# Optimization experiments

Measured on AMD Instinct MI355X. Metric: run time of the kernel, lower is better.

Reference implementation:

```python
import jax, jax.numpy as jnp
import numpy as np

B, T, D, H, L = 32, 512, 1024, 1024, 2


def setup_inputs() -> dict:
    key = jax.random.key(0)
    ks = jax.random.split(key, 8)
    s_in = 1.0 / np.sqrt(D)   # approximate orthogonal-init scale
    s_h = 1.0 / np.sqrt(H)
    return {
        "x": jax.random.normal(ks[0], (B, T, D), jnp.float32),
        "hidden": jnp.zeros((L, B, H), jnp.float32),
        "w_ih0": jax.random.normal(ks[1], (3 * H, D), jnp.float32) * s_in,
        "w_hh0": jax.random.normal(ks[2], (3 * H, H), jnp.float32) * s_h,
        "b_ih0": jnp.zeros((3 * H,), jnp.float32),
        "b_hh0": jnp.zeros((3 * H,), jnp.float32),
        "w_ih1": jax.random.normal(ks[3], (3 * H, H), jnp.float32) * s_h,
        "w_hh1": jax.random.normal(ks[4], (3 * H, H), jnp.float32) * s_h,
        "b_ih1": jnp.zeros((3 * H,), jnp.float32),
        "b_hh1": jnp.zeros((3 * H,), jnp.float32),
    }


def _gru_layer(x, h0, w_ih, w_hh, b_ih, b_hh):
    # x: [B,T,Din] -> precompute input projection once (as in source)
    xp = jnp.einsum('btd,gd->btg', x, w_ih) + b_ih        # [B,T,3H]
    xp_t = jnp.swapaxes(xp, 0, 1)                          # [T,B,3H]

    def step(h, xpt):
        hp = h @ w_hh.T + b_hh                             # [B,3H]
        r = jax.nn.sigmoid(xpt[:, :H] + hp[:, :H])
        z = jax.nn.sigmoid(xpt[:, H:2 * H] + hp[:, H:2 * H])
        n = jnp.tanh(xpt[:, 2 * H:] + r * hp[:, 2 * H:])
        h_new = (1 - z) * n + z * h
        return h_new, h_new

    h_last, ys = jax.lax.scan(step, h0, xp_t)              # ys: [T,B,H]
    return jnp.swapaxes(ys, 0, 1), h_last


def reference(x, hidden, w_ih0, w_hh0, b_ih0, b_hh0,
              w_ih1, w_hh1, b_ih1, b_hh1):
    y0, h0 = _gru_layer(x, hidden[0], w_ih0, w_hh0, b_ih0, b_hh0)
    y1, h1 = _gru_layer(y0, hidden[1], w_ih1, w_hh1, b_ih1, b_hh1)
    # dropout rates are 0.0 (eval semantics) -> identity
    return y1, jnp.stack([h0, h1], axis=0)
```

## Files before the change

kernel.cpp:

```cpp
#include <hip/hip_runtime.h>
#include <hip/hip_bf16.h>

#define NB 32
#define NT 512
#define NH 1024
#define G3 3072
#define NWG 128
#define PK_LDS (98304 + 16384 + 8192)

typedef __attribute__((ext_vector_type(8))) short short8;
typedef __attribute__((ext_vector_type(4))) float f32x4;
typedef __attribute__((ext_vector_type(4))) unsigned short us4;

static __device__ __forceinline__ unsigned short f2bf(float f) {
    union { float f; unsigned u; } v; v.f = f;
    if ((v.u & 0x7fffffffu) > 0x7f800000u) return (unsigned short)((v.u >> 16) | 0x0040u);
    unsigned u = v.u + 0x7fffu + ((v.u >> 16) & 1u);
    return (unsigned short)(u >> 16);
}

__global__ __launch_bounds__(256) void cvt_bf16_v4(const float4* __restrict__ src,
                                                   us4* __restrict__ dst, int n4) {
    for (int i = blockIdx.x * 256 + threadIdx.x; i < n4; i += gridDim.x * 256) {
        float4 v = src[i];
        us4 o;
        o.x = f2bf(v.x); o.y = f2bf(v.y); o.z = f2bf(v.z); o.w = f2bf(v.w);
        dst[i] = o;
    }
}

__global__ __launch_bounds__(256) void txp_x(const float4* __restrict__ x, us4* __restrict__ xt) {
    const int total = NT * NB * 256;
    for (int i = blockIdx.x * 256 + threadIdx.x; i < total; i += gridDim.x * 256) {
        int b = i / (NT * 256);
        int rem = i - b * (NT * 256);
        int t = rem >> 8;
        int d4 = rem & 255;
        float4 v = x[i];
        us4 o;
        o.x = f2bf(v.x); o.y = f2bf(v.y); o.z = f2bf(v.z); o.w = f2bf(v.w);
        xt[((size_t)t * NB + b) * 256 + d4] = o;
    }
}

__global__ __launch_bounds__(256) void init_h(const float* __restrict__ hid,
                                              float* __restrict__ h0f, unsigned short* __restrict__ h0b,
                                              float* __restrict__ h1f, unsigned short* __restrict__ h1b) {
    int i = blockIdx.x * 256 + threadIdx.x;
    float v0 = hid[i];
    float v1 = hid[NB * NH + i];
    h0f[i] = v0; h0b[i] = f2bf(v0);
    h1f[i] = v1; h1b[i] = f2bf(v1);
}

__global__ __launch_bounds__(256, 1) void gru_persistent(
    const unsigned short* __restrict__ xt,
    unsigned short* __restrict__ y0b,
    const unsigned short* __restrict__ wih0, const unsigned short* __restrict__ whh0,
    const unsigned short* __restrict__ wih1, const unsigned short* __restrict__ whh1,
    const float* __restrict__ bih0, const float* __restrict__ bhh0,
    const float* __restrict__ bih1, const float* __restrict__ bhh1,
    float* __restrict__ hf00, float* __restrict__ hf01,
    unsigned short* __restrict__ hb00, unsigned short* __restrict__ hb01,
    float* __restrict__ hf10, float* __restrict__ hf11,
    unsigned short* __restrict__ hb10, unsigned short* __restrict__ hb11,
    float* __restrict__ out,
    int* __restrict__ flags)
{
    extern __shared__ char lds[];
    short* blob = (short*)lds;
    float* part = (float*)(lds + 98304);
    float* hpf  = (float*)(lds + 98304 + 16384);

    const int tid  = threadIdx.x;
    const int lane = tid & 63;
    const int wv   = tid >> 6;
    const int kh   = wv & 1;
    const int mt   = wv >> 1;
    const int lr   = lane & 15;
    const int lq   = lane >> 4;

    const int wg   = blockIdx.x;
    const int lay  = wg >> 6;
    const int slot = wg & 63;
    const int j0   = slot * 16;

    int* fl0 = flags;
    int* fl1 = flags + 64 * 32;
    int* flown = lay ? fl1 : fl0;

    const unsigned short* wih = lay ? wih1 : wih0;
    const unsigned short* whh = lay ? whh1 : whh0;
    const float* bih = lay ? bih1 : bih0;
    const float* bhh = lay ? bhh1 : bhh0;
    float* hf[2]; unsigned short* hb[2];
    if (lay == 0) { hf[0] = hf00; hf[1] = hf01; hb[0] = hb00; hb[1] = hb01; }
    else          { hf[0] = hf10; hf[1] = hf11; hb[0] = hb10; hb[1] = hb11; }

    for (int c = tid; c < 6144; c += 256) {
        int g   = c >> 11;
        int rem = c & 2047;
        int kt  = rem >> 6;
        int q   = (rem >> 4) & 3;
        int col = rem & 15;
        *(short8*)(blob + c * 8) =
            *(const short8*)((const short*)whh + (size_t)(g * 1024 + j0 + col) * 1024 + kt * 32 + q * 8);
    }
    __syncthreads();

    const int aoff = (mt * 16 + lr) * 1024 + lq * 8;
    const short* wiB = (const short*)wih + (size_t)(j0 + lr) * 1024 + lq * 8;

    for (int t = 0; t < NT; ++t) {
        if (lay == 1) {
            if (wv == 0) {
                const int* p = fl0 + lane * 32;
                while (__hip_atomic_load(p, __ATOMIC_ACQUIRE, __HIP_MEMORY_SCOPE_AGENT) < t + 1)
                    __builtin_amdgcn_s_sleep(1);
            }
            __syncthreads();
        }

        const short* Asrc = lay ? (const short*)y0b : (const short*)xt;
        const short* Ap = Asrc + (size_t)t * NB * 1024 + aoff;

        f32x4 acc0 = {0.f,0.f,0.f,0.f};
        f32x4 acc1 = {0.f,0.f,0.f,0.f};
        f32x4 acc2 = {0.f,0.f,0.f,0.f};
        f32x4 acc3 = {0.f,0.f,0.f,0.f};

#pragma unroll 8
        for (int kk = 0; kk < 16; ++kk) {
            const int kt = kh * 16 + kk;
            short8 a  = *(const short8*)(Ap + kt * 32);
            short8 b0 = *(const short8*)(wiB + kt * 32);
            short8 b1 = *(const short8*)(wiB + 1024 * 1024 + kt * 32);
            short8 b2 = *(const short8*)(wiB + 2 * 1024 * 1024 + kt * 32);
            acc0 = __builtin_amdgcn_mfma_f32_16x16x32_bf16(a, b0, acc0, 0, 0, 0);
            acc1 = __builtin_amdgcn_mfma_f32_16x16x32_bf16(a, b1, acc1, 0, 0, 0);
            acc2 = __builtin_amdgcn_mfma_f32_16x16x32_bf16(a, b2, acc2, 0, 0, 0);
        }

        if (wv == 0) {
            const int* p = flown + lane * 32;
            while (__hip_atomic_load(p, __ATOMIC_ACQUIRE, __HIP_MEMORY_SCOPE_AGENT) < t)
                __builtin_amdgcn_s_sleep(1);
        }
        __syncthreads();

        const short* Ah = (const short*)hb[t & 1] + aoff;
#pragma unroll 8
        for (int kk = 0; kk < 16; ++kk) {
            const int kt = kh * 16 + kk;
            short8 a  = *(const short8*)(Ah + kt * 32);
            short8 c0 = *(const short8*)(blob + kt * 512 + lane * 8);
            short8 c1 = *(const short8*)(blob + (32 + kt) * 512 + lane * 8);
            short8 c2 = *(const short8*)(blob + (64 + kt) * 512 + lane * 8);
            acc0 = __builtin_amdgcn_mfma_f32_16x16x32_bf16(a, c0, acc0, 0, 0, 0);
            acc1 = __builtin_amdgcn_mfma_f32_16x16x32_bf16(a, c1, acc1, 0, 0, 0);
            acc3 = __builtin_amdgcn_mfma_f32_16x16x32_bf16(a, c2, acc3, 0, 0, 0);
        }

        *(f32x4*)(part + ((wv * 4 + 0) * 64 + lane) * 4) = acc0;
        *(f32x4*)(part + ((wv * 4 + 1) * 64 + lane) * 4) = acc1;
        *(f32x4*)(part + ((wv * 4 + 2) * 64 + lane) * 4) = acc2;
        *(f32x4*)(part + ((wv * 4 + 3) * 64 + lane) * 4) = acc3;
        __syncthreads();

        for (int eo = tid; eo < 2048; eo += 256) {
            int g2 = eo >> 9, b = (eo >> 4) & 31, c = eo & 15;
            int m = b >> 4, r = b & 3, l = ((b >> 2) & 3) * 16 + c;
            float v = part[(((m * 2 + 0) * 4 + g2) * 64 + l) * 4 + r]
                    + part[(((m * 2 + 1) * 4 + g2) * 64 + l) * 4 + r];
            hpf[eo] = v;
        }
        __syncthreads();

        float* hfin  = hf[t & 1];
        float* hfout = hf[(t + 1) & 1];
        unsigned short* hbout = hb[(t + 1) & 1];
        for (int e = tid; e < 512; e += 256) {
            int b = e >> 4, c = e & 15, gc = j0 + c;
            float pr  = hpf[e];
            float pz  = hpf[512 + e];
            float pxn = hpf[1024 + e];
            float phn = hpf[1536 + e];
            float r = 1.f / (1.f + __expf(-(pr + bih[gc] + bhh[gc])));
            float z = 1.f / (1.f + __expf(-(pz + bih[1024 + gc] + bhh[1024 + gc])));
            float n = tanhf(pxn + bih[2048 + gc] + r * (phn + bhh[2048 + gc]));
            float hprev = hfin[b * 1024 + gc];
            float hnew  = (1.f - z) * n + z * hprev;
            hfout[b * 1024 + gc] = hnew;
            hbout[b * 1024 + gc] = f2bf(hnew);
            if (lay == 0) y0b[((size_t)t * NB + b) * 1024 + gc] = f2bf(hnew);
            else          out[((size_t)b * NT + t) * 1024 + gc] = hnew;
            if (t == NT - 1)
                out[(size_t)NB * NT * 1024 + (size_t)lay * NB * 1024 + b * 1024 + gc] = hnew;
        }
        __syncthreads();

        if (tid == 0)
            __hip_atomic_store(flown + slot * 32, t + 1, __ATOMIC_RELEASE, __HIP_MEMORY_SCOPE_AGENT);
    }
}

extern "C" void kernel_launch(void* const* d_in, const int* in_sizes, int n_in,
                              void* d_out, int out_size, void* d_ws, size_t ws_size,
                              hipStream_t stream) {
    (void)in_sizes; (void)n_in; (void)out_size; (void)ws_size;

    const float* x     = (const float*)d_in[0];
    const float* hid   = (const float*)d_in[1];
    const float* w_ih0 = (const float*)d_in[2];
    const float* w_hh0 = (const float*)d_in[3];
    const float* b_ih0 = (const float*)d_in[4];
    const float* b_hh0 = (const float*)d_in[5];
    const float* w_ih1 = (const float*)d_in[6];
    const float* w_hh1 = (const float*)d_in[7];
    const float* b_ih1 = (const float*)d_in[8];
    const float* b_hh1 = (const float*)d_in[9];
    float* out = (float*)d_out;

    char* ws = (char*)d_ws;
    size_t off = 0;
    auto alloc = [&](size_t bytes) -> void* {
        void* p = ws + off;
        off += (bytes + 255) & ~(size_t)255;
        return p;
    };

    unsigned short* xtb   = (unsigned short*)alloc((size_t)NT * NB * 1024 * 2);
    unsigned short* y0b   = (unsigned short*)alloc((size_t)NT * NB * 1024 * 2);
    unsigned short* wih0b = (unsigned short*)alloc((size_t)G3 * 1024 * 2);
    unsigned short* whh0b = (unsigned short*)alloc((size_t)G3 * 1024 * 2);
    unsigned short* wih1b = (unsigned short*)alloc((size_t)G3 * 1024 * 2);
    unsigned short* whh1b = (unsigned short*)alloc((size_t)G3 * 1024 * 2);
    float*          hf0[2]; unsigned short* hb0[2];
    float*          hf1[2]; unsigned short* hb1[2];
    for (int i = 0; i < 2; i++) { hf0[i] = (float*)alloc(NB * NH * 4); hb0[i] = (unsigned short*)alloc(NB * NH * 2); }
    for (int i = 0; i < 2; i++) { hf1[i] = (float*)alloc(NB * NH * 4); hb1[i] = (unsigned short*)alloc(NB * NH * 2); }
    int* flags = (int*)alloc(2 * 64 * 32 * sizeof(int));

    txp_x<<<2048, 256, 0, stream>>>((const float4*)x, (us4*)xtb);
    cvt_bf16_v4<<<512, 256, 0, stream>>>((const float4*)w_ih0, (us4*)wih0b, G3 * 1024 / 4);
    cvt_bf16_v4<<<512, 256, 0, stream>>>((const float4*)w_hh0, (us4*)whh0b, G3 * 1024 / 4);
    cvt_bf16_v4<<<512, 256, 0, stream>>>((const float4*)w_ih1, (us4*)wih1b, G3 * 1024 / 4);
    cvt_bf16_v4<<<512, 256, 0, stream>>>((const float4*)w_hh1, (us4*)whh1b, G3 * 1024 / 4);
    init_h<<<NB * NH / 256, 256, 0, stream>>>(hid, hf0[0], hb0[0], hf1[0], hb1[0]);
    hipMemsetAsync(flags, 0, 2 * 64 * 32 * sizeof(int), stream);

    (void)hipFuncSetAttribute((const void*)gru_persistent,
                              hipFuncAttributeMaxDynamicSharedMemorySize, PK_LDS);
    gru_persistent<<<NWG, 256, PK_LDS, stream>>>(
        xtb, y0b, wih0b, whh0b, wih1b, whh1b,
        b_ih0, b_hh0, b_ih1, b_hh1,
        hf0[0], hf0[1], hb0[0], hb0[1],
        hf1[0], hf1[1], hb1[0], hb1[1],
        out, flags);
}
```

Measured before the change: 7.838 ms.

## Replace acquire/release flags with relaxed coherent loads and keep fp32 hidden state in LDS

Changes the cross-workgroup synchronization: the flag polls and store are now relaxed, and the data that other workgroups produce (the bf16 hidden state and y0) is read and written with relaxed agent-scope atomic 64-bit accesses plus an explicit vmcnt wait before the flag store. The intent is to avoid the cache invalidate and writeback that acquire/release fences cause every timestep. The fp32 previous hidden state for each workgroup's own slice now stays in LDS, so the global fp32 h buffers go away. Biases are preloaded into registers, and the gate update is vectorized over 4 columns per thread on 128 threads. The risk is memory-ordering correctness, since it depends on the relaxed atomics bypassing non-coherent caches.

```diff
diff --git a/kernel.cpp b/kernel.cpp
--- a/kernel.cpp
+++ b/kernel.cpp
@@ -6,17 +6,33 @@
 #define NH 1024
 #define G3 3072
 #define NWG 128
-#define PK_LDS (98304 + 16384 + 8192)
+#define LDS_BLOB 98304
+#define LDS_PART 16384
+#define LDS_HPF  8192
+#define LDS_HLOC 2048
+#define PK_LDS (LDS_BLOB + LDS_PART + LDS_HPF + LDS_HLOC)
 
 typedef __attribute__((ext_vector_type(8))) short short8;
 typedef __attribute__((ext_vector_type(4))) float f32x4;
 typedef __attribute__((ext_vector_type(4))) unsigned short us4;
+typedef unsigned long long u64;
 
 static __device__ __forceinline__ unsigned short f2bf(float f) {
     union { float f; unsigned u; } v; v.f = f;
     if ((v.u & 0x7fffffffu) > 0x7f800000u) return (unsigned short)((v.u >> 16) | 0x0040u);
     unsigned u = v.u + 0x7fffu + ((v.u >> 16) & 1u);
     return (unsigned short)(u >> 16);
+}
+
+static __device__ __forceinline__ short8 coh_load16(const u64* p) {
+    u64 lo = __hip_atomic_load(p,     __ATOMIC_RELAXED, __HIP_MEMORY_SCOPE_AGENT);
+    u64 hi = __hip_atomic_load(p + 1, __ATOMIC_RELAXED, __HIP_MEMORY_SCOPE_AGENT);
+    union { u64 u[2]; short8 s; } r;
+    r.u[0] = lo; r.u[1] = hi;
+    return r.s;
+}
+static __device__ __forceinline__ void coh_store8(u64* p, u64 v) {
+    __hip_atomic_store(p, v, __ATOMIC_RELAXED, __HIP_MEMORY_SCOPE_AGENT);
 }
 
 __global__ __launch_bounds__(256) void cvt_bf16_v4(const float4* __restrict__ src,
@@ -44,13 +60,11 @@
 }
 
 __global__ __launch_bounds__(256) void init_h(const float* __restrict__ hid,
-                                              float* __restrict__ h0f, unsigned short* __restrict__ h0b,
-                                              float* __restrict__ h1f, unsigned short* __restrict__ h1b) {
+                                              unsigned short* __restrict__ h0b,
+                                              unsigned short* __restrict__ h1b) {
     int i = blockIdx.x * 256 + threadIdx.x;
-    float v0 = hid[i];
-    float v1 = hid[NB * NH + i];
-    h0f[i] = v0; h0b[i] = f2bf(v0);
-    h1f[i] = v1; h1b[i] = f2bf(v1);
+    h0b[i] = f2bf(hid[i]);
+    h1b[i] = f2bf(hid[NB * NH + i]);
 }
 
 __global__ __launch_bounds__(256, 1) void gru_persistent(
@@ -60,17 +74,17 @@
     const unsigned short* __restrict__ wih1, const unsigned short* __restrict__ whh1,
     const float* __restrict__ bih0, const float* __restrict__ bhh0,
     const float* __restrict__ bih1, const float* __restrict__ bhh1,
-    float* __restrict__ hf00, float* __restrict__ hf01,
+    const float* __restrict__ hid,
     unsigned short* __restrict__ hb00, unsigned short* __restrict__ hb01,
-    float* __restrict__ hf10, float* __restrict__ hf11,
     unsigned short* __restrict__ hb10, unsigned short* __restrict__ hb11,
     float* __restrict__ out,
     int* __restrict__ flags)
 {
     extern __shared__ char lds[];
     short* blob = (short*)lds;
-    float* part = (float*)(lds + 98304);
-    float* hpf  = (float*)(lds + 98304 + 16384);
+    float* part = (float*)(lds + LDS_BLOB);
+    float* hpf  = (float*)(lds + LDS_BLOB + LDS_PART);
+    float* hloc = (float*)(lds + LDS_BLOB + LDS_PART + LDS_HPF);
 
     const int tid  = threadIdx.x;
     const int lane = tid & 63;
@@ -85,17 +99,16 @@
     const int slot = wg & 63;
     const int j0   = slot * 16;
 
-    int* fl0 = flags;
-    int* fl1 = flags + 64 * 32;
-    int* flown = lay ? fl1 : fl0;
+    int* fl0   = flags;
+    int* flown = lay ? (flags + 64 * 32) : flags;
 
     const unsigned short* wih = lay ? wih1 : wih0;
     const unsigned short* whh = lay ? whh1 : whh0;
     const float* bih = lay ? bih1 : bih0;
     const float* bhh = lay ? bhh1 : bhh0;
-    float* hf[2]; unsigned short* hb[2];
-    if (lay == 0) { hf[0] = hf00; hf[1] = hf01; hb[0] = hb00; hb[1] = hb01; }
-    else          { hf[0] = hf10; hf[1] = hf11; hb[0] = hb10; hb[1] = hb11; }
+    unsigned short* hb[2];
+    if (lay == 0) { hb[0] = hb00; hb[1] = hb01; }
+    else          { hb[0] = hb10; hb[1] = hb11; }
 
     for (int c = tid; c < 6144; c += 256) {
         int g   = c >> 11;
@@ -106,6 +119,21 @@
         *(short8*)(blob + c * 8) =
             *(const short8*)((const short*)whh + (size_t)(g * 1024 + j0 + col) * 1024 + kt * 32 + q * 8);
     }
+
+    float br_[4], bz_[4], bxn_[4], bhn_[4];
+    if (tid < 128) {
+        const int b = tid >> 2, c4 = (tid & 3) * 4;
+#pragma unroll
+        for (int j = 0; j < 4; ++j) {
+            int gc = j0 + c4 + j;
+            br_[j]  = bih[gc] + bhh[gc];
+            bz_[j]  = bih[1024 + gc] + bhh[1024 + gc];
+            bxn_[j] = bih[2048 + gc];
+            bhn_[j] = bhh[2048 + gc];
+        }
+        float4 h0 = *(const float4*)&hid[(size_t)lay * NB * NH + (size_t)b * 1024 + j0 + c4];
+        *(float4*)&hloc[b * 16 + c4] = h0;
+    }
     __syncthreads();
 
     const int aoff = (mt * 16 + lr) * 1024 + lq * 8;
@@ -115,50 +143,67 @@
         if (lay == 1) {
             if (wv == 0) {
                 const int* p = fl0 + lane * 32;
-                while (__hip_atomic_load(p, __ATOMIC_ACQUIRE, __HIP_MEMORY_SCOPE_AGENT) < t + 1)
+                while (__hip_atomic_load(p, __ATOMIC_RELAXED, __HIP_MEMORY_SCOPE_AGENT) < t + 1)
                     __builtin_amdgcn_s_sleep(1);
             }
+            asm volatile("" ::: "memory");
             __syncthreads();
         }
-
-        const short* Asrc = lay ? (const short*)y0b : (const short*)xt;
-        const short* Ap = Asrc + (size_t)t * NB * 1024 + aoff;
 
         f32x4 acc0 = {0.f,0.f,0.f,0.f};
         f32x4 acc1 = {0.f,0.f,0.f,0.f};
         f32x4 acc2 = {0.f,0.f,0.f,0.f};
         f32x4 acc3 = {0.f,0.f,0.f,0.f};
 
+        if (lay == 0) {
+            const short* Ap = (const short*)xt + (size_t)t * NB * 1024 + aoff;
 #pragma unroll 8
-        for (int kk = 0; kk < 16; ++kk) {
-            const int kt = kh * 16 + kk;
-            short8 a  = *(const short8*)(Ap + kt * 32);
-            short8 b0 = *(const short8*)(wiB + kt * 32);
-            short8 b1 = *(const short8*)(wiB + 1024 * 1024 + kt * 32);
-            short8 b2 = *(const short8*)(wiB + 2 * 1024 * 1024 + kt * 32);
-            acc0 = __builtin_amdgcn_mfma_f32_16x16x32_bf16(a, b0, acc0, 0, 0, 0);
-            acc1 = __builtin_amdgcn_mfma_f32_16x16x32_bf16(a, b1, acc1, 0, 0, 0);
-            acc2 = __builtin_amdgcn_mfma_f32_16x16x32_bf16(a, b2, acc2, 0, 0, 0);
+            for (int kk = 0; kk < 16; ++kk) {
+                const int kt = kh * 16 + kk;
+                short8 a  = *(const short8*)(Ap + kt * 32);
+                short8 b0 = *(const short8*)(wiB + kt * 32);
+                short8 b1 = *(const short8*)(wiB + 1024 * 1024 + kt * 32);
+                short8 b2 = *(const short8*)(wiB + 2 * 1024 * 1024 + kt * 32);
+                acc0 = __builtin_amdgcn_mfma_f32_16x16x32_bf16(a, b0, acc0, 0, 0, 0);
+                acc1 = __builtin_amdgcn_mfma_f32_16x16x32_bf16(a, b1, acc1, 0, 0, 0);
+                acc2 = __builtin_amdgcn_mfma_f32_16x16x32_bf16(a, b2, acc2, 0, 0, 0);
+            }
+        } else {
+            const u64* Ap = (const u64*)((const short*)y0b + (size_t)t * NB * 1024 + aoff);
+#pragma unroll 8
+            for (int kk = 0; kk < 16; ++kk) {
+                const int kt = kh * 16 + kk;
+                short8 a  = coh_load16(Ap + kt * 8);
+                short8 b0 = *(const short8*)(wiB + kt * 32);
+                short8 b1 = *(const short8*)(wiB + 1024 * 1024 + kt * 32);
+                short8 b2 = *(const short8*)(wiB + 2 * 1024 * 1024 + kt * 32);
+                acc0 = __builtin_amdgcn_mfma_f32_16x16x32_bf16(a, b0, acc0, 0, 0, 0);
+                acc1 = __builtin_amdgcn_mfma_f32_16x16x32_bf16(a, b1, acc1, 0, 0, 0);
+                acc2 = __builtin_amdgcn_mfma_f32_16x16x32_bf16(a, b2, acc2, 0, 0, 0);
+            }
         }
 
         if (wv == 0) {
             const int* p = flown + lane * 32;
-            while (__hip_atomic_load(p, __ATOMIC_ACQUIRE, __HIP_MEMORY_SCOPE_AGENT) < t)
+            while (__hip_atomic_load(p, __ATOMIC_RELAXED, __HIP_MEMORY_SCOPE_AGENT) < t)
                 __builtin_amdgcn_s_sleep(1);
         }
+        asm volatile("" ::: "memory");
         __syncthreads();
 
-        const short* Ah = (const short*)hb[t & 1] + aoff;
+        {
+            const u64* Hb = (const u64*)((const short*)hb[t & 1] + aoff);
 #pragma unroll 8
-        for (int kk = 0; kk < 16; ++kk) {
-            const int kt = kh * 16 + kk;
-            short8 a  = *(const short8*)(Ah + kt * 32);
-            short8 c0 = *(const short8*)(blob + kt * 512 + lane * 8);
-            short8 c1 = *(const short8*)(blob + (32 + kt) * 512 + lane * 8);
-            short8 c2 = *(const short8*)(blob + (64 + kt) * 512 + lane * 8);
-            acc0 = __builtin_amdgcn_mfma_f32_16x16x32_bf16(a, c0, acc0, 0, 0, 0);
-            acc1 = __builtin_amdgcn_mfma_f32_16x16x32_bf16(a, c1, acc1, 0, 0, 0);
-            acc3 = __builtin_amdgcn_mfma_f32_16x16x32_bf16(a, c2, acc3, 0, 0, 0);
+            for (int kk = 0; kk < 16; ++kk) {
+                const int kt = kh * 16 + kk;
+                short8 a  = coh_load16(Hb + kt * 8);
+                short8 c0 = *(const short8*)(blob + kt * 512 + lane * 8);
+                short8 c1 = *(const short8*)(blob + (32 + kt) * 512 + lane * 8);
+                short8 c2 = *(const short8*)(blob + (64 + kt) * 512 + lane * 8);
+                acc0 = __builtin_amdgcn_mfma_f32_16x16x32_bf16(a, c0, acc0, 0, 0, 0);
+                acc1 = __builtin_amdgcn_mfma_f32_16x16x32_bf16(a, c1, acc1, 0, 0, 0);
+                acc3 = __builtin_amdgcn_mfma_f32_16x16x32_bf16(a, c2, acc3, 0, 0, 0);
+            }
         }
 
         *(f32x4*)(part + ((wv * 4 + 0) * 64 + lane) * 4) = acc0;
@@ -176,31 +221,44 @@
         }
         __syncthreads();
 
-        float* hfin  = hf[t & 1];
-        float* hfout = hf[(t + 1) & 1];
-        unsigned short* hbout = hb[(t + 1) & 1];
-        for (int e = tid; e < 512; e += 256) {
-            int b = e >> 4, c = e & 15, gc = j0 + c;
-            float pr  = hpf[e];
-            float pz  = hpf[512 + e];
-            float pxn = hpf[1024 + e];
-            float phn = hpf[1536 + e];
-            float r = 1.f / (1.f + __expf(-(pr + bih[gc] + bhh[gc])));
-            float z = 1.f / (1.f + __expf(-(pz + bih[1024 + gc] + bhh[1024 + gc])));
-            float n = tanhf(pxn + bih[2048 + gc] + r * (phn + bhh[2048 + gc]));
-            float hprev = hfin[b * 1024 + gc];
-            float hnew  = (1.f - z) * n + z * hprev;
-            hfout[b * 1024 + gc] = hnew;
-            hbout[b * 1024 + gc] = f2bf(hnew);
-            if (lay == 0) y0b[((size_t)t * NB + b) * 1024 + gc] = f2bf(hnew);
-            else          out[((size_t)b * NT + t) * 1024 + gc] = hnew;
-            if (t == NT - 1)
-                out[(size_t)NB * NT * 1024 + (size_t)lay * NB * 1024 + b * 1024 + gc] = hnew;
-        }
+        if (tid < 128) {
+            const int b = tid >> 2, c4 = (tid & 3) * 4;
+            const int gc0 = j0 + c4;
+            float hn[4];
+            u64 hpack = 0;
+#pragma unroll
+            for (int j = 0; j < 4; ++j) {
+                const int e = b * 16 + c4 + j;
+                float pr  = hpf[e];
+                float pz  = hpf[512 + e];
+                float pxn = hpf[1024 + e];
+                float phn = hpf[1536 + e];
+                float r = 1.f / (1.f + __expf(-(pr + br_[j])));
+                float z = 1.f / (1.f + __expf(-(pz + bz_[j])));
+                float n = tanhf(pxn + bxn_[j] + r * (phn + bhn_[j]));
+                float hprev = hloc[e];
+                float h = (1.f - z) * n + z * hprev;
+                hloc[e] = h;
+                hn[j] = h;
+                hpack |= (u64)f2bf(h) << (16 * j);
+            }
+            coh_store8((u64*)((unsigned short*)hb[(t + 1) & 1] + (size_t)b * 1024 + gc0), hpack);
+            if (lay == 0) {
+                coh_store8((u64*)(y0b + ((size_t)t * NB + b) * 1024 + gc0), hpack);
+            } else {
+                float4 o4; o4.x = hn[0]; o4.y = hn[1]; o4.z = hn[2]; o4.w = hn[3];
+                *(float4*)&out[((size_t)b * NT + t) * 1024 + gc0] = o4;
+            }
+            if (t == NT - 1) {
+                float4 o4; o4.x = hn[0]; o4.y = hn[1]; o4.z = hn[2]; o4.w = hn[3];
+                *(float4*)&out[(size_t)NB * NT * 1024 + (size_t)lay * NB * NH + (size_t)b * 1024 + gc0] = o4;
+            }
+        }
+
+        asm volatile("s_waitcnt vmcnt(0)" ::: "memory");
         __syncthreads();
-
         if (tid == 0)
-            __hip_atomic_store(flown + slot * 32, t + 1, __ATOMIC_RELEASE, __HIP_MEMORY_SCOPE_AGENT);
+            __hip_atomic_store(flown + slot * 32, t + 1, __ATOMIC_RELAXED, __HIP_MEMORY_SCOPE_AGENT);
     }
 }
 
@@ -235,10 +293,9 @@
     unsigned short* whh0b = (unsigned short*)alloc((size_t)G3 * 1024 * 2);
     unsigned short* wih1b = (unsigned short*)alloc((size_t)G3 * 1024 * 2);
     unsigned short* whh1b = (unsigned short*)alloc((size_t)G3 * 1024 * 2);
-    float*          hf0[2]; unsigned short* hb0[2];
-    float*          hf1[2]; unsigned short* hb1[2];
-    for (int i = 0; i < 2; i++) { hf0[i] = (float*)alloc(NB * NH * 4); hb0[i] = (unsigned short*)alloc(NB * NH * 2); }
-    for (int i = 0; i < 2; i++) { hf1[i] = (float*)alloc(NB * NH * 4); hb1[i] = (unsigned short*)alloc(NB * NH * 2); }
+    unsigned short* hb0[2]; unsigned short* hb1[2];
+    for (int i = 0; i < 2; i++) hb0[i] = (unsigned short*)alloc(NB * NH * 2);
+    for (int i = 0; i < 2; i++) hb1[i] = (unsigned short*)alloc(NB * NH * 2);
     int* flags = (int*)alloc(2 * 64 * 32 * sizeof(int));
 
     txp_x<<<2048, 256, 0, stream>>>((const float4*)x, (us4*)xtb);
@@ -246,15 +303,14 @@
     cvt_bf16_v4<<<512, 256, 0, stream>>>((const float4*)w_hh0, (us4*)whh0b, G3 * 1024 / 4);
     cvt_bf16_v4<<<512, 256, 0, stream>>>((const float4*)w_ih1, (us4*)wih1b, G3 * 1024 / 4);
     cvt_bf16_v4<<<512, 256, 0, stream>>>((const float4*)w_hh1, (us4*)whh1b, G3 * 1024 / 4);
-    init_h<<<NB * NH / 256, 256, 0, stream>>>(hid, hf0[0], hb0[0], hf1[0], hb1[0]);
+    init_h<<<NB * NH / 256, 256, 0, stream>>>(hid, hb0[0], hb1[0]);
     hipMemsetAsync(flags, 0, 2 * 64 * 32 * sizeof(int), stream);
 
     (void)hipFuncSetAttribute((const void*)gru_persistent,
                               hipFuncAttributeMaxDynamicSharedMemorySize, PK_LDS);
     gru_persistent<<<NWG, 256, PK_LDS, stream>>>(
         xtb, y0b, wih0b, whh0b, wih1b, whh1b,
-        b_ih0, b_hh0, b_ih1, b_hh1,
-        hf0[0], hf0[1], hb0[0], hb0[1],
-        hf1[0], hf1[1], hb1[0], hb1[1],
+        b_ih0, b_hh0, b_ih1, b_hh1, hid,
+        hb0[0], hb0[1], hb1[0], hb1[1],
         out, flags);
 }
```

After: 8.378 ms. +6.9%, slower.
